# Optimization experiments

Measured on AMD Instinct MI355X. Metric: run time of the kernel, lower is better.

## Reference

```python
import jax, jax.numpy as jnp
import numpy as np

IN_DIM = 128
OUT_DIM = 128
ATTN_DIM = 64
N_REL = 200
N_NODE = 50000
N_EDGE = 500000
N_QUERY = 64
COE_TIMEDIFF = 0.2  # computed in torch code but unused downstream


def setup_inputs() -> dict:
    key = jax.random.key(0)
    ks = jax.random.split(key, 24)
    # edges: [E,7] with columns (r_idx, _, rel, _, tau, sub, obj)
    r_idx = jax.random.randint(ks[0], (N_EDGE,), 0, N_QUERY)
    rel = jax.random.randint(ks[1], (N_EDGE,), 0, 2 * N_REL + 1)
    tau = jax.random.randint(ks[2], (N_EDGE,), -1, 366)  # -1 triggers the where() fallback
    sub = jax.random.randint(ks[3], (N_EDGE,), 0, N_NODE)
    obj = jax.random.randint(ks[4], (N_EDGE,), 0, N_NODE)
    fill = jnp.zeros((N_EDGE,), jnp.int64 if jax.config.jax_enable_x64 else jnp.int32)
    edges = jnp.stack([r_idx, fill, rel, fill, tau, sub, obj], axis=1)
    s = 1.0 / np.sqrt(IN_DIM)
    sa = 1.0 / np.sqrt(ATTN_DIM)
    return {
        "q_sub": jax.random.randint(ks[5], (N_QUERY,), 0, N_NODE),
        "q_rel": jax.random.randint(ks[6], (N_QUERY,), 0, 2 * N_REL + 1),
        "q_tau": jax.random.randint(ks[7], (N_QUERY,), 0, 366),
        "hidden": jax.random.normal(ks[8], (N_NODE, IN_DIM), jnp.float32),
        "edges": edges,
        "n_node": N_NODE,
        "old_nodes_new_idx": jax.random.randint(ks[9], (10000,), 0, N_NODE),
        "rela_embed": jax.random.normal(ks[10], (2 * N_REL + 1, IN_DIM), jnp.float32),
        "Ws": jax.random.normal(ks[11], (IN_DIM, ATTN_DIM), jnp.float32) * s,
        "Wr": jax.random.normal(ks[12], (IN_DIM, ATTN_DIM), jnp.float32) * s,
        "Wqr_W": jax.random.normal(ks[13], (IN_DIM, ATTN_DIM), jnp.float32) * s,
        "Wqr_b": jax.random.normal(ks[14], (ATTN_DIM,), jnp.float32) * s,
        "Wtau": jax.random.normal(ks[15], (IN_DIM, ATTN_DIM), jnp.float32) * s,
        "w_alpha_W": jax.random.normal(ks[16], (ATTN_DIM, 1), jnp.float32) * sa,
        "w_alpha_b": jax.random.normal(ks[17], (1,), jnp.float32) * sa,
        "Wh": jax.random.normal(ks[18], (IN_DIM, OUT_DIM), jnp.float32) * s,
        "wt1": jax.random.normal(ks[19], (1, IN_DIM), jnp.float32),
        "bt1": jax.random.normal(ks[20], (1, IN_DIM), jnp.float32),
        "wt2": jax.random.normal(ks[21], (1, IN_DIM), jnp.float32),
        "bt2": jax.random.normal(ks[22], (1, IN_DIM), jnp.float32),
    }


def reference(q_sub, q_rel, q_tau, hidden, edges, n_node, old_nodes_new_idx,
              rela_embed, Ws, Wr, Wqr_W, Wqr_b, Wtau, w_alpha_W, w_alpha_b,
              Wh, wt1, bt1, wt2, bt2):
    r_idx = edges[:, 0]
    rel = edges[:, 2]
    tau = edges[:, 4]
    sub = edges[:, 5]
    obj = edges[:, 6]
    hs = hidden[sub]                      # [E, in_dim] gather
    hr = rela_embed[rel]                  # [E, in_dim]
    h_qr = rela_embed[q_rel][r_idx]       # [E, in_dim]
    taus_q = q_tau[r_idx]
    tau = jnp.where(tau >= 0, tau, taus_q)
    delta_tau = (tau - taus_q).astype(hidden.dtype)[:, None]  # [E,1]
    h_tau = wt1 * delta_tau + bt1 + jnp.sin(wt2 * delta_tau + bt2)  # [E, in_dim]
    message = hs + hr + h_tau
    pre = jax.nn.relu(hs @ Ws + hr @ Wr + (h_qr @ Wqr_W + Wqr_b) + h_tau @ Wtau)
    alpha = jax.nn.sigmoid(pre @ w_alpha_W + w_alpha_b)  # [E,1]
    msg_agg = jax.ops.segment_sum(alpha * message, obj, num_segments=n_node)
    return msg_agg @ Wh  # act is identity by default
```

## Files before the change

kernel.cpp:

```cpp
#include <hip/hip_runtime.h>
#include <hip/hip_fp16.h>

#define IN_DIM   128
#define OUT_DIM  128
#define ATTN_DIM 64
#define N_RELV   401
#define N_NODE   50000
#define N_EDGE   500000
#define N_QUERY  64
#define N_DT     731
#define CAP      40

typedef unsigned short ushort_t;
typedef unsigned int   uint_t;
typedef __attribute__((ext_vector_type(8))) short v8s;
typedef __attribute__((ext_vector_type(4))) float v4f;

__device__ __forceinline__ int clampi(int v, int lo, int hi) {
    return v < lo ? lo : (v > hi ? hi : v);
}
__device__ __forceinline__ float bu2f(ushort_t u) {
    union { uint_t i; float f; } v; v.i = ((uint_t)u) << 16; return v.f;
}
__device__ __forceinline__ float blo(uint_t u) { return bu2f((ushort_t)(u & 0xffff)); }
__device__ __forceinline__ float bhi(uint_t u) { return bu2f((ushort_t)(u >> 16)); }
__device__ __forceinline__ ushort_t f2bu(float f) {
    union { float f; uint_t i; } v; v.f = f;
    const uint_t x = v.i;
    return (ushort_t)((x + 0x7fffu + ((x >> 16) & 1u)) >> 16);
}

__device__ __forceinline__ void parse_edge(const int* __restrict__ edges, int e,
                                           int i64, int& r, int& rel, int& tau,
                                           int& sub, int& obj) {
    if (i64) {
        const int* E = edges + (size_t)e * 14;
        r = E[0]; rel = E[4]; tau = E[8]; sub = E[10]; obj = E[12];
    } else {
        const int* E = edges + (size_t)e * 7;
        r = E[0]; rel = E[2]; tau = E[4]; sub = E[5]; obj = E[6];
    }
    r   = clampi(r,   0, N_QUERY - 1);
    rel = clampi(rel, 0, N_RELV - 1);
    sub = clampi(sub, 0, N_NODE - 1);
    obj = clampi(obj, 0, N_NODE - 1);
}

__global__ __launch_bounds__(256) void prep_kernel(
    const int* __restrict__ edges, const float* __restrict__ Ws,
    const float* __restrict__ Wh, ushort_t* __restrict__ WTb,
    int* __restrict__ flag, int* __restrict__ cnt, int* __restrict__ ovfn)
{
    const int i = blockIdx.x * 256 + threadIdx.x;
    const int n = i >> 7, k = i & 127;
    const float w = (n < 64) ? Ws[k * 64 + n] : Wh[k * 128 + (n - 64)];
    WTb[i] = f2bu(w);

    for (int idx = i; idx < N_NODE; idx += 96 * 256) cnt[idx] = 0;
    if (i == 0) ovfn[0] = 0;

    if (blockIdx.x == 0) {
        __shared__ int bad;
        if (threadIdx.x == 0) bad = 0;
        __syncthreads();
        for (int t = threadIdx.x; t < 1000; t += 256) {
            const int w32 = edges[2 * t + 1];
            if (w32 != 0 && w32 != -1) bad = 1;
        }
        __syncthreads();
        if (threadIdx.x == 0) flag[0] = (bad == 0) ? 1 : 0;
    }
}

__global__ __launch_bounds__(256) void node_tab_mfma(
    const float* __restrict__ hidden, const ushort_t* __restrict__ WTb,
    ushort_t* __restrict__ node_attn, ushort_t* __restrict__ node_msg)
{
    const int tid  = threadIdx.x;
    const int wid  = tid >> 6;
    const int lane = tid & 63;
    const int m16  = lane & 15;
    const int q    = lane >> 4;
    const int nb   = blockIdx.x * 64;
    const int row  = nb + wid * 16 + m16;
    const int rowc = row < N_NODE ? row : N_NODE - 1;

    v8s hfr[4];
    #pragma unroll
    for (int c = 0; c < 4; ++c) {
        const float4 f0 = *(const float4*)(hidden + (size_t)rowc * 128 + 32 * c + 8 * q);
        const float4 f1 = *(const float4*)(hidden + (size_t)rowc * 128 + 32 * c + 8 * q + 4);
        v8s a;
        a[0] = (short)f2bu(f0.x); a[1] = (short)f2bu(f0.y);
        a[2] = (short)f2bu(f0.z); a[3] = (short)f2bu(f0.w);
        a[4] = (short)f2bu(f1.x); a[5] = (short)f2bu(f1.y);
        a[6] = (short)f2bu(f1.z); a[7] = (short)f2bu(f1.w);
        hfr[c] = a;
    }

    #pragma unroll
    for (int t = 0; t < 12; ++t) {
        v4f acc = {0.f, 0.f, 0.f, 0.f};
        #pragma unroll
        for (int c = 0; c < 4; ++c) {
            const v8s wfr = *(const v8s*)(WTb + (size_t)(16 * t + m16) * 128 + 32 * c + 8 * q);
            acc = __builtin_amdgcn_mfma_f32_16x16x32_bf16(wfr, hfr[c], acc, 0, 0, 0);
        }
        if (row < N_NODE) {
            const uint_t u0 = (uint_t)f2bu(acc[0]) | ((uint_t)f2bu(acc[1]) << 16);
            const uint_t u1 = (uint_t)f2bu(acc[2]) | ((uint_t)f2bu(acc[3]) << 16);
            const int dim = 16 * t + 4 * q;
            if (dim < 64) {
                uint2* dst = (uint2*)(node_attn + (size_t)row * 64 + dim);
                *dst = make_uint2(u0, u1);
            } else {
                uint2* dst = (uint2*)(node_msg + (size_t)row * 128 + (dim - 64));
                *dst = make_uint2(u0, u1);
            }
        }
    }
}

__global__ __launch_bounds__(128) void tables_kernel(
    const float* __restrict__ rela, const float* __restrict__ Wr,
    const float* __restrict__ Wtau, const float* __restrict__ Wh,
    const float* __restrict__ wt1, const float* __restrict__ bt1,
    const float* __restrict__ wt2, const float* __restrict__ bt2,
    const int* __restrict__ q_rel, const float* __restrict__ WqrW,
    const float* __restrict__ Wqrb, const int* __restrict__ flag,
    ushort_t* __restrict__ rel_attn, ushort_t* __restrict__ rel_msg,
    ushort_t* __restrict__ dt_attn,  ushort_t* __restrict__ dt_msg,
    ushort_t* __restrict__ Xqr)
{
    const int b = blockIdx.x, tid = threadIdx.x;
    __shared__ float h[IN_DIM];

    if (b < N_RELV) {
        const int r = b;
        h[tid] = rela[(size_t)r * IN_DIM + tid];
        __syncthreads();
        if (tid < ATTN_DIM) {
            float a = 0.f;
            #pragma unroll 8
            for (int d = 0; d < IN_DIM; ++d) a += h[d] * Wr[d * ATTN_DIM + tid];
            rel_attn[(size_t)r * ATTN_DIM + tid] = f2bu(a);
        }
        float m = 0.f;
        #pragma unroll 8
        for (int d = 0; d < IN_DIM; ++d) m += h[d] * Wh[d * OUT_DIM + tid];
        rel_msg[(size_t)r * OUT_DIM + tid] = f2bu(m);
    } else if (b < N_RELV + N_DT) {
        const int i = b - N_RELV;
        const float dt = (float)(i - 365);
        h[tid] = wt1[tid] * dt + bt1[tid] + sinf(wt2[tid] * dt + bt2[tid]);
        __syncthreads();
        if (tid < ATTN_DIM) {
            float a = 0.f;
            #pragma unroll 8
            for (int d = 0; d < IN_DIM; ++d) a += h[d] * Wtau[d * ATTN_DIM + tid];
            dt_attn[(size_t)i * ATTN_DIM + tid] = f2bu(a);
        }
        float m = 0.f;
        #pragma unroll 8
        for (int d = 0; d < IN_DIM; ++d) m += h[d] * Wh[d * OUT_DIM + tid];
        dt_msg[(size_t)i * OUT_DIM + tid] = f2bu(m);
    } else {
        const int qn  = b - N_RELV - N_DT;
        const int i64 = flag[0];
        const int rel = clampi(q_rel[i64 ? 2 * qn : qn], 0, N_RELV - 1);
        h[tid] = rela[(size_t)rel * IN_DIM + tid];
        __syncthreads();
        if (tid < ATTN_DIM) {
            float acc = Wqrb[tid];
            #pragma unroll 8
            for (int d = 0; d < IN_DIM; ++d) acc += h[d] * WqrW[d * ATTN_DIM + tid];
            Xqr[(size_t)qn * ATTN_DIM + tid] = f2bu(acc);
        }
    }
}

__device__ __forceinline__ float dot8(uint4 xs, uint4 xr, uint4 xt, uint4 xq,
                                      float4 wA, float4 wB)
{
    float s0, s1, v;
    s0 = blo(xs.x) + blo(xr.x) + blo(xt.x) + blo(xq.x);
    s1 = bhi(xs.x) + bhi(xr.x) + bhi(xt.x) + bhi(xq.x);
    v  = fmaxf(s0, 0.f) * wA.x + fmaxf(s1, 0.f) * wA.y;
    s0 = blo(xs.y) + blo(xr.y) + blo(xt.y) + blo(xq.y);
    s1 = bhi(xs.y) + bhi(xr.y) + bhi(xt.y) + bhi(xq.y);
    v += fmaxf(s0, 0.f) * wA.z + fmaxf(s1, 0.f) * wA.w;
    s0 = blo(xs.z) + blo(xr.z) + blo(xt.z) + blo(xq.z);
    s1 = bhi(xs.z) + bhi(xr.z) + bhi(xt.z) + bhi(xq.z);
    v += fmaxf(s0, 0.f) * wB.x + fmaxf(s1, 0.f) * wB.y;
    s0 = blo(xs.w) + blo(xr.w) + blo(xt.w) + blo(xq.w);
    s1 = bhi(xs.w) + bhi(xr.w) + bhi(xt.w) + bhi(xq.w);
    v += fmaxf(s0, 0.f) * wB.z + fmaxf(s1, 0.f) * wB.w;
    return v;
}

__global__ __launch_bounds__(256) void alpha_scatter(
    const int* __restrict__ edges, const int* __restrict__ q_tau,
    const ushort_t* __restrict__ node_attn, const ushort_t* __restrict__ rel_attn,
    const ushort_t* __restrict__ dt_attn,  const ushort_t* __restrict__ Xqr,
    const float* __restrict__ w_alpha_W, const float* __restrict__ w_alpha_b,
    const int* __restrict__ flag, int* __restrict__ cnt,
    int2* __restrict__ meta, int* __restrict__ ovfn, int4* __restrict__ ovfl)
{
    const int g   = threadIdx.x & 7;
    const int grp = threadIdx.x >> 3;
    const int e0  = blockIdx.x * 64 + grp * 2;
    const int i64 = flag[0];

    const float4 wA = *(const float4*)(w_alpha_W + 8 * g);
    const float4 wB = *(const float4*)(w_alpha_W + 8 * g + 4);

    const int ea = e0     < N_EDGE ? e0     : N_EDGE - 1;
    const int eb = e0 + 1 < N_EDGE ? e0 + 1 : N_EDGE - 1;

    int r0, rel0, tau0, sub0, obj0, r1, rel1, tau1, sub1, obj1;
    parse_edge(edges, ea, i64, r0, rel0, tau0, sub0, obj0);
    parse_edge(edges, eb, i64, r1, rel1, tau1, sub1, obj1);
    const int tq0 = q_tau[i64 ? 2 * r0 : r0];
    const int tq1 = q_tau[i64 ? 2 * r1 : r1];
    if (tau0 < 0) tau0 = tq0;
    if (tau1 < 0) tau1 = tq1;
    const int di0 = clampi(tau0 - tq0 + 365, 0, N_DT - 1);
    const int di1 = clampi(tau1 - tq1 + 365, 0, N_DT - 1);

    const uint4 xs0 = *(const uint4*)(node_attn + (size_t)sub0 * ATTN_DIM + 8 * g);
    const uint4 xr0 = *(const uint4*)(rel_attn + (size_t)rel0 * ATTN_DIM + 8 * g);
    const uint4 xt0 = *(const uint4*)(dt_attn  + (size_t)di0  * ATTN_DIM + 8 * g);
    const uint4 xq0 = *(const uint4*)(Xqr      + (size_t)r0   * ATTN_DIM + 8 * g);
    const uint4 xs1 = *(const uint4*)(node_attn + (size_t)sub1 * ATTN_DIM + 8 * g);
    const uint4 xr1 = *(const uint4*)(rel_attn + (size_t)rel1 * ATTN_DIM + 8 * g);
    const uint4 xt1 = *(const uint4*)(dt_attn  + (size_t)di1  * ATTN_DIM + 8 * g);
    const uint4 xq1 = *(const uint4*)(Xqr      + (size_t)r1   * ATTN_DIM + 8 * g);

    float v0 = dot8(xs0, xr0, xt0, xq0, wA, wB);
    float v1 = dot8(xs1, xr1, xt1, xq1, wA, wB);
    v0 += __shfl_down(v0, 4, 8);
    v1 += __shfl_down(v1, 4, 8);
    v0 += __shfl_down(v0, 2, 8);
    v1 += __shfl_down(v1, 2, 8);
    v0 += __shfl_down(v0, 1, 8);
    v1 += __shfl_down(v1, 1, 8);

    if (g == 0) {
        const float wb = w_alpha_b[0];
        if (e0 < N_EDGE) {
            const float alpha = 1.f / (1.f + __expf(-(v0 + wb)));
            const int pos = atomicAdd(&cnt[obj0], 1);
            if (pos < CAP) {
                const uint_t px = (uint_t)sub0 | ((uint_t)di0 << 17) | ((uint_t)(rel0 & 31) << 27);
                const uint_t py = (uint_t)(rel0 >> 5) |
                                  ((uint_t)__half_as_ushort(__float2half_rn(alpha)) << 16);
                meta[(size_t)obj0 * CAP + pos] = make_int2((int)px, (int)py);
            } else {
                const int ov = atomicAdd(ovfn, 1);
                if (ov < N_EDGE)
                    ovfl[ov] = make_int4(sub0 | (di0 << 17), rel0 | (obj0 << 9),
                                         __float_as_int(alpha), 0);
            }
        }
        if (e0 + 1 < N_EDGE) {
            const float alpha = 1.f / (1.f + __expf(-(v1 + wb)));
            const int pos = atomicAdd(&cnt[obj1], 1);
            if (pos < CAP) {
                const uint_t px = (uint_t)sub1 | ((uint_t)di1 << 17) | ((uint_t)(rel1 & 31) << 27);
                const uint_t py = (uint_t)(rel1 >> 5) |
                                  ((uint_t)__half_as_ushort(__float2half_rn(alpha)) << 16);
                meta[(size_t)obj1 * CAP + pos] = make_int2((int)px, (int)py);
            } else {
                const int ov = atomicAdd(ovfn, 1);
                if (ov < N_EDGE)
                    ovfl[ov] = make_int4(sub1 | (di1 << 17), rel1 | (obj1 << 9),
                                         __float_as_int(alpha), 0);
            }
        }
    }
}

__device__ __forceinline__ void meta_decode(int2 m, int& sub, int& di, int& rel,
                                            float& al)
{
    sub = m.x & 0x1FFFF;
    di  = ((uint_t)m.x >> 17) & 0x3FF;
    rel = (((uint_t)m.x >> 27) & 31) | (((uint_t)m.y & 0xF) << 5);
    al  = __half2float(__ushort_as_half((ushort_t)((uint_t)m.y >> 16)));
}

__global__ __launch_bounds__(256) void agg_kernel(
    const int* __restrict__ cnt, const int2* __restrict__ meta,
    const int* __restrict__ ovfn, const int4* __restrict__ ovfl,
    const ushort_t* __restrict__ node_msg, const ushort_t* __restrict__ rel_msg,
    const ushort_t* __restrict__ dt_msg, float* __restrict__ out)
{
    const int lane = threadIdx.x & 63;
    const int n    = blockIdx.x * 4 + (threadIdx.x >> 6);

    int m = cnt[n]; if (m > CAP) m = CAP;
    const int2* row = meta + (size_t)n * CAP;
    float a0 = 0.f, a1 = 0.f;
    int j = 0;
    for (; j + 3 < m; j += 4) {
        const int2 m0 = row[j], m1 = row[j + 1], m2 = row[j + 2], m3 = row[j + 3];
        int s0, d0, r0; float w0; meta_decode(m0, s0, d0, r0, w0);
        int s1, d1, r1; float w1; meta_decode(m1, s1, d1, r1, w1);
        int s2, d2, r2; float w2; meta_decode(m2, s2, d2, r2, w2);
        int s3, d3, r3; float w3; meta_decode(m3, s3, d3, r3, w3);
        const uint_t am0 = *(const uint_t*)(node_msg + (size_t)s0 * 128 + 2 * lane);
        const uint_t bm0 = *(const uint_t*)(rel_msg  + (size_t)r0 * 128 + 2 * lane);
        const uint_t tm0 = *(const uint_t*)(dt_msg   + (size_t)d0 * 128 + 2 * lane);
        const uint_t am1 = *(const uint_t*)(node_msg + (size_t)s1 * 128 + 2 * lane);
        const uint_t bm1 = *(const uint_t*)(rel_msg  + (size_t)r1 * 128 + 2 * lane);
        const uint_t tm1 = *(const uint_t*)(dt_msg   + (size_t)d1 * 128 + 2 * lane);
        const uint_t am2 = *(const uint_t*)(node_msg + (size_t)s2 * 128 + 2 * lane);
        const uint_t bm2 = *(const uint_t*)(rel_msg  + (size_t)r2 * 128 + 2 * lane);
        const uint_t tm2 = *(const uint_t*)(dt_msg   + (size_t)d2 * 128 + 2 * lane);
        const uint_t am3 = *(const uint_t*)(node_msg + (size_t)s3 * 128 + 2 * lane);
        const uint_t bm3 = *(const uint_t*)(rel_msg  + (size_t)r3 * 128 + 2 * lane);
        const uint_t tm3 = *(const uint_t*)(dt_msg   + (size_t)d3 * 128 + 2 * lane);
        a0 += w0 * (blo(am0) + blo(bm0) + blo(tm0));
        a1 += w0 * (bhi(am0) + bhi(bm0) + bhi(tm0));
        a0 += w1 * (blo(am1) + blo(bm1) + blo(tm1));
        a1 += w1 * (bhi(am1) + bhi(bm1) + bhi(tm1));
        a0 += w2 * (blo(am2) + blo(bm2) + blo(tm2));
        a1 += w2 * (bhi(am2) + bhi(bm2) + bhi(tm2));
        a0 += w3 * (blo(am3) + blo(bm3) + blo(tm3));
        a1 += w3 * (bhi(am3) + bhi(bm3) + bhi(tm3));
    }
    for (; j < m; ++j) {
        const int2 m0 = row[j];
        int s0, d0, r0; float w0; meta_decode(m0, s0, d0, r0, w0);
        const uint_t am0 = *(const uint_t*)(node_msg + (size_t)s0 * 128 + 2 * lane);
        const uint_t bm0 = *(const uint_t*)(rel_msg  + (size_t)r0 * 128 + 2 * lane);
        const uint_t tm0 = *(const uint_t*)(dt_msg   + (size_t)d0 * 128 + 2 * lane);
        a0 += w0 * (blo(am0) + blo(bm0) + blo(tm0));
        a1 += w0 * (bhi(am0) + bhi(bm0) + bhi(tm0));
    }

    int nov = ovfn[0]; if (nov > N_EDGE) nov = N_EDGE;
    for (int i = 0; i < nov; ++i) {
        const int4 mo = ovfl[i];
        const int objo = (int)((uint_t)mo.y >> 9);
        if (objo != n) continue;
        const int subo = mo.x & 0x1FFFF;
        const int dio  = (int)((uint_t)mo.x >> 17);
        const int relo = mo.y & 0x1FF;
        const float alo = __int_as_float(mo.z);
        const uint_t am = *(const uint_t*)(node_msg + (size_t)subo * 128 + 2 * lane);
        const uint_t bm = *(const uint_t*)(rel_msg  + (size_t)relo * 128 + 2 * lane);
        const uint_t tm = *(const uint_t*)(dt_msg   + (size_t)dio  * 128 + 2 * lane);
        a0 += alo * (blo(am) + blo(bm) + blo(tm));
        a1 += alo * (bhi(am) + bhi(bm) + bhi(tm));
    }

    ((float2*)(out + (size_t)n * OUT_DIM))[lane] = make_float2(a0, a1);
}

__global__ __launch_bounds__(256) void edge_atomic_kernel(
    const int* __restrict__ edges, const int* __restrict__ q_tau,
    const ushort_t* __restrict__ node_attn, const ushort_t* __restrict__ node_msg,
    const ushort_t* __restrict__ rel_attn,  const ushort_t* __restrict__ rel_msg,
    const ushort_t* __restrict__ dt_attn,   const ushort_t* __restrict__ dt_msg,
    const ushort_t* __restrict__ Xqr,
    const float* __restrict__ w_alpha_W, const float* __restrict__ w_alpha_b,
    const int* __restrict__ flag, float* __restrict__ out)
{
    const int lane = threadIdx.x & 63;
    const int e    = blockIdx.x * 4 + (threadIdx.x >> 6);
    const int i64  = flag[0];

    int r, rel, tau, sub, obj;
    parse_edge(edges, e, i64, r, rel, tau, sub, obj);
    const int tq = q_tau[i64 ? 2 * r : r];
    if (tau < 0) tau = tq;
    const int di = clampi(tau - tq + 365, 0, N_DT - 1);

    const float xs = bu2f(node_attn[(size_t)sub * ATTN_DIM + lane]);
    const float xr = bu2f(rel_attn[(size_t)rel * ATTN_DIM + lane]);
    const float xt = bu2f(dt_attn[(size_t)di  * ATTN_DIM + lane]);
    const float xq = bu2f(Xqr[(size_t)r * ATTN_DIM + lane]);

    float v = fmaxf(xs + xr + xq + xt, 0.f) * w_alpha_W[lane];
    #pragma unroll
    for (int off = 32; off > 0; off >>= 1)
        v += __shfl_down(v, off, 64);
    v = __shfl(v, 0, 64);
    const float alpha = 1.f / (1.f + __expf(-(v + w_alpha_b[0])));

    const uint_t am = *(const uint_t*)(node_msg + (size_t)sub * 128 + 2 * lane);
    const uint_t bm = *(const uint_t*)(rel_msg  + (size_t)rel * 128 + 2 * lane);
    const uint_t tm = *(const uint_t*)(dt_msg   + (size_t)di  * 128 + 2 * lane);
    const float mx = blo(am) + blo(bm) + blo(tm);
    const float my = bhi(am) + bhi(bm) + bhi(tm);

    float* dst = out + (size_t)obj * OUT_DIM;
    atomicAdd(dst + 2 * lane,     alpha * mx);
    atomicAdd(dst + 2 * lane + 1, alpha * my);
}

extern "C" void kernel_launch(void* const* d_in, const int* in_sizes, int n_in,
                              void* d_out, int out_size, void* d_ws, size_t ws_size,
                              hipStream_t stream)
{
    const int*   q_rel  = (const int*)d_in[1];
    const int*   q_tau  = (const int*)d_in[2];
    const float* hidden = (const float*)d_in[3];
    const int*   edges  = (const int*)d_in[4];
    const float* rela   = (const float*)d_in[7];
    const float* Ws     = (const float*)d_in[8];
    const float* Wr     = (const float*)d_in[9];
    const float* WqrW   = (const float*)d_in[10];
    const float* Wqrb   = (const float*)d_in[11];
    const float* Wtau   = (const float*)d_in[12];
    const float* waW    = (const float*)d_in[13];
    const float* wab    = (const float*)d_in[14];
    const float* Wh     = (const float*)d_in[15];
    const float* wt1    = (const float*)d_in[16];
    const float* bt1    = (const float*)d_in[17];
    const float* wt2    = (const float*)d_in[18];
    const float* bt2    = (const float*)d_in[19];
    float* out = (float*)d_out;

    char* p = (char*)d_ws;
    size_t off = 0;
    auto carve = [&](size_t bytes) {
        char* q = p + off;
        off = (off + bytes + 255) & ~(size_t)255;
        return q;
    };
    int*      flag      = (int*)     carve(64);
    int*      cnt       = (int*)     carve((size_t)N_NODE * 4);
    int*      ovfn      = (int*)     carve(64);
    ushort_t* WTb       = (ushort_t*)carve((size_t)192 * 128 * 2);
    ushort_t* XqrB      = (ushort_t*)carve((size_t)N_QUERY * ATTN_DIM * 2);
    ushort_t* rel_attn  = (ushort_t*)carve((size_t)N_RELV * ATTN_DIM * 2);
    ushort_t* rel_msg   = (ushort_t*)carve((size_t)N_RELV * OUT_DIM * 2);
    ushort_t* dt_attn   = (ushort_t*)carve((size_t)N_DT * ATTN_DIM * 2);
    ushort_t* dt_msg    = (ushort_t*)carve((size_t)N_DT * OUT_DIM * 2);
    ushort_t* node_attn = (ushort_t*)carve((size_t)N_NODE * ATTN_DIM * 2);
    ushort_t* node_msg  = (ushort_t*)carve((size_t)N_NODE * OUT_DIM * 2);
    int2*     meta      = (int2*)    carve((size_t)N_NODE * CAP * 8);
    int4*     ovfl      = (int4*)    carve((size_t)N_EDGE * 16);
    const size_t need_full = off;

    prep_kernel<<<96, 256, 0, stream>>>(edges, Ws, Wh, WTb, flag, cnt, ovfn);
    tables_kernel<<<N_RELV + N_DT + N_QUERY, 128, 0, stream>>>(
        rela, Wr, Wtau, Wh, wt1, bt1, wt2, bt2, q_rel, WqrW, Wqrb, flag,
        rel_attn, rel_msg, dt_attn, dt_msg, XqrB);
    node_tab_mfma<<<(N_NODE + 63) / 64, 256, 0, stream>>>(hidden, WTb,
                                                          node_attn, node_msg);

    if (ws_size >= need_full) {
        alpha_scatter<<<(N_EDGE + 63) / 64, 256, 0, stream>>>(
            edges, q_tau, node_attn, rel_attn, dt_attn, XqrB,
            waW, wab, flag, cnt, meta, ovfn, ovfl);
        agg_kernel<<<N_NODE / 4, 256, 0, stream>>>(cnt, meta, ovfn, ovfl,
                                                   node_msg, rel_msg, dt_msg, out);
    } else {
        (void)hipMemsetAsync(out, 0, (size_t)out_size * sizeof(float), stream);
        edge_atomic_kernel<<<N_EDGE / 4, 256, 0, stream>>>(edges, q_tau,
                                                           node_attn, node_msg,
                                                           rel_attn, rel_msg,
                                                           dt_attn, dt_msg, XqrB,
                                                           waW, wab, flag, out);
    }
}
```

Before: 217.1 us.

## Fuse preprocessing kernels, transpose meta layout, widen edge and aggregation work per thread

```diff
diff --git a/kernel.cpp b/kernel.cpp
--- a/kernel.cpp
+++ b/kernel.cpp
@@ -11,6 +11,11 @@
 #define N_DT     731
 #define CAP      40
 
+#define NB_NODE  782
+#define NB_RELDT 566
+#define NB_QR    32
+#define NB_TOT   (NB_NODE + NB_RELDT + NB_QR + 1)
+
 typedef unsigned short ushort_t;
 typedef unsigned int   uint_t;
 typedef __attribute__((ext_vector_type(8))) short v8s;
@@ -28,6 +33,11 @@
     union { float f; uint_t i; } v; v.f = f;
     const uint_t x = v.i;
     return (ushort_t)((x + 0x7fffu + ((x >> 16) & 1u)) >> 16);
+}
+__device__ __forceinline__ uint_t cvtpk(float a, float b) {
+    uint_t r;
+    asm("v_cvt_pk_bf16_f32 %0, %1, %2" : "=v"(r) : "v"(a), "v"(b));
+    return r;
 }
 
 __device__ __forceinline__ void parse_edge(const int* __restrict__ edges, int e,
@@ -46,136 +56,178 @@
     obj = clampi(obj, 0, N_NODE - 1);
 }
 
-__global__ __launch_bounds__(256) void prep_kernel(
-    const int* __restrict__ edges, const float* __restrict__ Ws,
-    const float* __restrict__ Wh, ushort_t* __restrict__ WTb,
+__device__ __forceinline__ int swz_byte(int row, int byte_in_row) {
+    return (row * 256 + byte_in_row) ^ ((row & 7) << 4);
+}
+
+__global__ __launch_bounds__(256) void fused_pre(
+    const float* __restrict__ hidden, const float* __restrict__ Ws,
+    const float* __restrict__ Wh,   const float* __restrict__ rela,
+    const float* __restrict__ Wr,   const float* __restrict__ Wtau,
+    const float* __restrict__ wt1,  const float* __restrict__ bt1,
+    const float* __restrict__ wt2,  const float* __restrict__ bt2,
+    const int* __restrict__ q_rel,  const float* __restrict__ WqrW,
+    const float* __restrict__ Wqrb, const int* __restrict__ edges,
+    ushort_t* __restrict__ node_attn, ushort_t* __restrict__ node_msg,
+    ushort_t* __restrict__ rel_attn,  ushort_t* __restrict__ rel_msg,
+    ushort_t* __restrict__ dt_attn,   ushort_t* __restrict__ dt_msg,
+    ushort_t* __restrict__ Xqr,
     int* __restrict__ flag, int* __restrict__ cnt, int* __restrict__ ovfn)
 {
-    const int i = blockIdx.x * 256 + threadIdx.x;
-    const int n = i >> 7, k = i & 127;
-    const float w = (n < 64) ? Ws[k * 64 + n] : Wh[k * 128 + (n - 64)];
-    WTb[i] = f2bu(w);
-
-    for (int idx = i; idx < N_NODE; idx += 96 * 256) cnt[idx] = 0;
-    if (i == 0) ovfn[0] = 0;
-
-    if (blockIdx.x == 0) {
-        __shared__ int bad;
-        if (threadIdx.x == 0) bad = 0;
-        __syncthreads();
-        for (int t = threadIdx.x; t < 1000; t += 256) {
-            const int w32 = edges[2 * t + 1];
-            if (w32 != 0 && w32 != -1) bad = 1;
-        }
-        __syncthreads();
-        if (threadIdx.x == 0) flag[0] = (bad == 0) ? 1 : 0;
-    }
-}
-
-__global__ __launch_bounds__(256) void node_tab_mfma(
-    const float* __restrict__ hidden, const ushort_t* __restrict__ WTb,
-    ushort_t* __restrict__ node_attn, ushort_t* __restrict__ node_msg)
-{
-    const int tid  = threadIdx.x;
-    const int wid  = tid >> 6;
-    const int lane = tid & 63;
-    const int m16  = lane & 15;
-    const int q    = lane >> 4;
-    const int nb   = blockIdx.x * 64;
-    const int row  = nb + wid * 16 + m16;
-    const int rowc = row < N_NODE ? row : N_NODE - 1;
-
-    v8s hfr[4];
-    #pragma unroll
-    for (int c = 0; c < 4; ++c) {
-        const float4 f0 = *(const float4*)(hidden + (size_t)rowc * 128 + 32 * c + 8 * q);
-        const float4 f1 = *(const float4*)(hidden + (size_t)rowc * 128 + 32 * c + 8 * q + 4);
-        v8s a;
-        a[0] = (short)f2bu(f0.x); a[1] = (short)f2bu(f0.y);
-        a[2] = (short)f2bu(f0.z); a[3] = (short)f2bu(f0.w);
-        a[4] = (short)f2bu(f1.x); a[5] = (short)f2bu(f1.y);
-        a[6] = (short)f2bu(f1.z); a[7] = (short)f2bu(f1.w);
-        hfr[c] = a;
-    }
-
-    #pragma unroll
-    for (int t = 0; t < 12; ++t) {
-        v4f acc = {0.f, 0.f, 0.f, 0.f};
+    __shared__ ushort_t shw[192 * 128];
+    const int bid = blockIdx.x, tid = threadIdx.x;
+
+    if (bid < NB_NODE) {
+        #pragma unroll
+        for (int i = 0; i < 4; ++i) {
+            const int pi = tid + 256 * i;
+            const int kp = pi >> 4;
+            const int n4 = (pi & 15) * 4;
+            const float4 A = *(const float4*)(Ws + (size_t)(2 * kp) * 64 + n4);
+            const float4 B = *(const float4*)(Ws + (size_t)(2 * kp + 1) * 64 + n4);
+            const float Aa[4] = {A.x, A.y, A.z, A.w};
+            const float Bа[4] = {B.x, B.y, B.z, B.w};
+            #pragma unroll
+            for (int j = 0; j < 4; ++j) {
+                const int row = n4 + j;
+                const uint_t u = (uint_t)f2bu(Aa[j]) | ((uint_t)f2bu(Bа[j]) << 16);
+                *(uint_t*)((char*)shw + swz_byte(row, kp * 4)) = u;
+            }
+        }
+        #pragma unroll
+        for (int i = 0; i < 8; ++i) {
+            const int pi = tid + 256 * i;
+            const int kp = pi >> 5;
+            const int n4 = (pi & 31) * 4;
+            const float4 A = *(const float4*)(Wh + (size_t)(2 * kp) * 128 + n4);
+            const float4 B = *(const float4*)(Wh + (size_t)(2 * kp + 1) * 128 + n4);
+            const float Aa[4] = {A.x, A.y, A.z, A.w};
+            const float Bа[4] = {B.x, B.y, B.z, B.w};
+            #pragma unroll
+            for (int j = 0; j < 4; ++j) {
+                const int row = 64 + n4 + j;
+                const uint_t u = (uint_t)f2bu(Aa[j]) | ((uint_t)f2bu(Bа[j]) << 16);
+                *(uint_t*)((char*)shw + swz_byte(row, kp * 4)) = u;
+            }
+        }
+        __syncthreads();
+
+        const int wid  = tid >> 6;
+        const int lane = tid & 63;
+        const int m16  = lane & 15;
+        const int q    = lane >> 4;
+        const int nb   = bid * 64;
+        const int row  = nb + wid * 16 + m16;
+        const int rowc = row < N_NODE ? row : N_NODE - 1;
+
+        v8s hfr[4];
         #pragma unroll
         for (int c = 0; c < 4; ++c) {
-            const v8s wfr = *(const v8s*)(WTb + (size_t)(16 * t + m16) * 128 + 32 * c + 8 * q);
-            acc = __builtin_amdgcn_mfma_f32_16x16x32_bf16(wfr, hfr[c], acc, 0, 0, 0);
-        }
-        if (row < N_NODE) {
-            const uint_t u0 = (uint_t)f2bu(acc[0]) | ((uint_t)f2bu(acc[1]) << 16);
-            const uint_t u1 = (uint_t)f2bu(acc[2]) | ((uint_t)f2bu(acc[3]) << 16);
-            const int dim = 16 * t + 4 * q;
-            if (dim < 64) {
-                uint2* dst = (uint2*)(node_attn + (size_t)row * 64 + dim);
-                *dst = make_uint2(u0, u1);
-            } else {
-                uint2* dst = (uint2*)(node_msg + (size_t)row * 128 + (dim - 64));
-                *dst = make_uint2(u0, u1);
+            const float4 f0 = *(const float4*)(hidden + (size_t)rowc * 128 + 32 * c + 8 * q);
+            const float4 f1 = *(const float4*)(hidden + (size_t)rowc * 128 + 32 * c + 8 * q + 4);
+            union { v8s s; uint4 u; } uu;
+            uu.u = make_uint4(cvtpk(f0.x, f0.y), cvtpk(f0.z, f0.w),
+                              cvtpk(f1.x, f1.y), cvtpk(f1.z, f1.w));
+            hfr[c] = uu.s;
+        }
+
+        #pragma unroll
+        for (int t = 0; t < 12; ++t) {
+            v4f acc = {0.f, 0.f, 0.f, 0.f};
+            #pragma unroll
+            for (int c = 0; c < 4; ++c) {
+                const v8s wfr = *(const v8s*)((const char*)shw +
+                                  swz_byte(16 * t + m16, (32 * c + 8 * q) * 2));
+                acc = __builtin_amdgcn_mfma_f32_16x16x32_bf16(wfr, hfr[c], acc, 0, 0, 0);
             }
-        }
-    }
-}
-
-__global__ __launch_bounds__(128) void tables_kernel(
-    const float* __restrict__ rela, const float* __restrict__ Wr,
-    const float* __restrict__ Wtau, const float* __restrict__ Wh,
-    const float* __restrict__ wt1, const float* __restrict__ bt1,
-    const float* __restrict__ wt2, const float* __restrict__ bt2,
-    const int* __restrict__ q_rel, const float* __restrict__ WqrW,
-    const float* __restrict__ Wqrb, const int* __restrict__ flag,
-    ushort_t* __restrict__ rel_attn, ushort_t* __restrict__ rel_msg,
-    ushort_t* __restrict__ dt_attn,  ushort_t* __restrict__ dt_msg,
-    ushort_t* __restrict__ Xqr)
-{
-    const int b = blockIdx.x, tid = threadIdx.x;
-    __shared__ float h[IN_DIM];
-
-    if (b < N_RELV) {
-        const int r = b;
-        h[tid] = rela[(size_t)r * IN_DIM + tid];
-        __syncthreads();
-        if (tid < ATTN_DIM) {
-            float a = 0.f;
+            if (row < N_NODE) {
+                const uint_t u0 = cvtpk(acc[0], acc[1]);
+                const uint_t u1 = cvtpk(acc[2], acc[3]);
+                const int dim = 16 * t + 4 * q;
+                if (dim < 64) {
+                    *(uint2*)(node_attn + (size_t)row * 64 + dim) = make_uint2(u0, u1);
+                } else {
+                    *(uint2*)(node_msg + (size_t)row * 128 + (dim - 64)) = make_uint2(u0, u1);
+                }
+            }
+        }
+    } else if (bid < NB_NODE + NB_RELDT) {
+        const int bid2   = bid - NB_NODE;
+        const int half   = tid >> 7;
+        const int t128   = tid & 127;
+        const int rowid  = bid2 * 2 + half;
+        float* h = (float*)shw + half * 128;
+
+        if (rowid < N_RELV) {
+            h[t128] = rela[(size_t)rowid * IN_DIM + t128];
+        } else {
+            const float dtv = (float)((rowid - N_RELV) - 365);
+            h[t128] = wt1[t128] * dtv + bt1[t128] + sinf(wt2[t128] * dtv + bt2[t128]);
+        }
+        __syncthreads();
+
+        if (rowid < N_RELV) {
+            if (t128 < ATTN_DIM) {
+                float a = 0.f;
+                #pragma unroll 8
+                for (int d = 0; d < IN_DIM; ++d) a += h[d] * Wr[d * ATTN_DIM + t128];
+                rel_attn[(size_t)rowid * ATTN_DIM + t128] = f2bu(a);
+            }
+            float m = 0.f;
             #pragma unroll 8
-            for (int d = 0; d < IN_DIM; ++d) a += h[d] * Wr[d * ATTN_DIM + tid];
-            rel_attn[(size_t)r * ATTN_DIM + tid] = f2bu(a);
-        }
-        float m = 0.f;
-        #pragma unroll 8
-        for (int d = 0; d < IN_DIM; ++d) m += h[d] * Wh[d * OUT_DIM + tid];
-        rel_msg[(size_t)r * OUT_DIM + tid] = f2bu(m);
-    } else if (b < N_RELV + N_DT) {
-        const int i = b - N_RELV;
-        const float dt = (float)(i - 365);
-        h[tid] = wt1[tid] * dt + bt1[tid] + sinf(wt2[tid] * dt + bt2[tid]);
-        __syncthreads();
-        if (tid < ATTN_DIM) {
-            float a = 0.f;
+            for (int d = 0; d < IN_DIM; ++d) m += h[d] * Wh[d * OUT_DIM + t128];
+            rel_msg[(size_t)rowid * OUT_DIM + t128] = f2bu(m);
+        } else {
+            const int i = rowid - N_RELV;
+            if (t128 < ATTN_DIM) {
+                float a = 0.f;
+                #pragma unroll 8
+                for (int d = 0; d < IN_DIM; ++d) a += h[d] * Wtau[d * ATTN_DIM + t128];
+                dt_attn[(size_t)i * ATTN_DIM + t128] = f2bu(a);
+            }
+            float m = 0.f;
             #pragma unroll 8
-            for (int d = 0; d < IN_DIM; ++d) a += h[d] * Wtau[d * ATTN_DIM + tid];
-            dt_attn[(size_t)i * ATTN_DIM + tid] = f2bu(a);
-        }
-        float m = 0.f;
-        #pragma unroll 8
-        for (int d = 0; d < IN_DIM; ++d) m += h[d] * Wh[d * OUT_DIM + tid];
-        dt_msg[(size_t)i * OUT_DIM + tid] = f2bu(m);
+            for (int d = 0; d < IN_DIM; ++d) m += h[d] * Wh[d * OUT_DIM + t128];
+            dt_msg[(size_t)i * OUT_DIM + t128] = f2bu(m);
+        }
+        const int z = bid2 * 89 + tid;
+        if (tid < 89 && z < N_NODE) cnt[z] = 0;
+    } else if (bid < NB_NODE + NB_RELDT + NB_QR) {
+        const int bid3 = bid - NB_NODE - NB_RELDT;
+        const int half = tid >> 7;
+        const int t128 = tid & 127;
+        float* h  = (float*)shw + half * 128;
+        int*   ok = (int*)((float*)shw + 512);
+
+        if (tid == 0) *ok = 1;
+        __syncthreads();
+        const int w = edges[2 * tid + 1];
+        if (w != 0 && w != -1) *ok = 0;
+        __syncthreads();
+        const int i64 = *ok;
+
+        const int qn  = bid3 * 2 + half;
+        const int rel = clampi(q_rel[i64 ? 2 * qn : qn], 0, N_RELV - 1);
+        h[t128] = rela[(size_t)rel * IN_DIM + t128];
+        __syncthreads();
+        if (t128 < ATTN_DIM) {
+            float acc = Wqrb[t128];
+            #pragma unroll 8
+            for (int d = 0; d < IN_DIM; ++d) acc += h[d] * WqrW[d * ATTN_DIM + t128];
+            Xqr[(size_t)qn * ATTN_DIM + t128] = f2bu(acc);
+        }
     } else {
-        const int qn  = b - N_RELV - N_DT;
-        const int i64 = flag[0];
-        const int rel = clampi(q_rel[i64 ? 2 * qn : qn], 0, N_RELV - 1);
-        h[tid] = rela[(size_t)rel * IN_DIM + tid];
-        __syncthreads();
-        if (tid < ATTN_DIM) {
-            float acc = Wqrb[tid];
-            #pragma unroll 8
-            for (int d = 0; d < IN_DIM; ++d) acc += h[d] * WqrW[d * ATTN_DIM + tid];
-            Xqr[(size_t)qn * ATTN_DIM + tid] = f2bu(acc);
-        }
+        int* ok = (int*)shw;
+        if (tid == 0) *ok = 0;
+        __syncthreads();
+        int badv = 0;
+        for (int t = tid; t < 1000; t += 256) {
+            const int w = edges[2 * t + 1];
+            if (w != 0 && w != -1) badv = 1;
+        }
+        if (badv) *ok = 1;
+        __syncthreads();
+        if (tid == 0) { flag[0] = (*ok == 0) ? 1 : 0; ovfn[0] = 0; }
     }
 }
 
@@ -208,24 +260,33 @@
 {
     const int g   = threadIdx.x & 7;
     const int grp = threadIdx.x >> 3;
-    const int e0  = blockIdx.x * 64 + grp * 2;
+    const int e0  = blockIdx.x * 128 + grp * 4;
     const int i64 = flag[0];
 
     const float4 wA = *(const float4*)(w_alpha_W + 8 * g);
     const float4 wB = *(const float4*)(w_alpha_W + 8 * g + 4);
 
-    const int ea = e0     < N_EDGE ? e0     : N_EDGE - 1;
-    const int eb = e0 + 1 < N_EDGE ? e0 + 1 : N_EDGE - 1;
-
-    int r0, rel0, tau0, sub0, obj0, r1, rel1, tau1, sub1, obj1;
-    parse_edge(edges, ea, i64, r0, rel0, tau0, sub0, obj0);
-    parse_edge(edges, eb, i64, r1, rel1, tau1, sub1, obj1);
+    const int ec0 = e0     < N_EDGE ? e0     : N_EDGE - 1;
+    const int ec1 = e0 + 1 < N_EDGE ? e0 + 1 : N_EDGE - 1;
+    const int ec2 = e0 + 2 < N_EDGE ? e0 + 2 : N_EDGE - 1;
+    const int ec3 = e0 + 3 < N_EDGE ? e0 + 3 : N_EDGE - 1;
+
+    int r0, rel0, tau0, sub0, obj0; parse_edge(edges, ec0, i64, r0, rel0, tau0, sub0, obj0);
+    int r1, rel1, tau1, sub1, obj1; parse_edge(edges, ec1, i64, r1, rel1, tau1, sub1, obj1);
+    int r2, rel2, tau2, sub2, obj2; parse_edge(edges, ec2, i64, r2, rel2, tau2, sub2, obj2);
+    int r3, rel3, tau3, sub3, obj3; parse_edge(edges, ec3, i64, r3, rel3, tau3, sub3, obj3);
     const int tq0 = q_tau[i64 ? 2 * r0 : r0];
     const int tq1 = q_tau[i64 ? 2 * r1 : r1];
+    const int tq2 = q_tau[i64 ? 2 * r2 : r2];
+    const int tq3 = q_tau[i64 ? 2 * r3 : r3];
     if (tau0 < 0) tau0 = tq0;
     if (tau1 < 0) tau1 = tq1;
+    if (tau2 < 0) tau2 = tq2;
+    if (tau3 < 0) tau3 = tq3;
     const int di0 = clampi(tau0 - tq0 + 365, 0, N_DT - 1);
     const int di1 = clampi(tau1 - tq1 + 365, 0, N_DT - 1);
+    const int di2 = clampi(tau2 - tq2 + 365, 0, N_DT - 1);
+    const int di3 = clampi(tau3 - tq3 + 365, 0, N_DT - 1);
 
     const uint4 xs0 = *(const uint4*)(node_attn + (size_t)sub0 * ATTN_DIM + 8 * g);
     const uint4 xr0 = *(const uint4*)(rel_attn + (size_t)rel0 * ATTN_DIM + 8 * g);
@@ -235,58 +296,67 @@
     const uint4 xr1 = *(const uint4*)(rel_attn + (size_t)rel1 * ATTN_DIM + 8 * g);
     const uint4 xt1 = *(const uint4*)(dt_attn  + (size_t)di1  * ATTN_DIM + 8 * g);
     const uint4 xq1 = *(const uint4*)(Xqr      + (size_t)r1   * ATTN_DIM + 8 * g);
+    const uint4 xs2 = *(const uint4*)(node_attn + (size_t)sub2 * ATTN_DIM + 8 * g);
+    const uint4 xr2 = *(const uint4*)(rel_attn + (size_t)rel2 * ATTN_DIM + 8 * g);
+    const uint4 xt2 = *(const uint4*)(dt_attn  + (size_t)di2  * ATTN_DIM + 8 * g);
+    const uint4 xq2 = *(const uint4*)(Xqr      + (size_t)r2   * ATTN_DIM + 8 * g);
+    const uint4 xs3 = *(const uint4*)(node_attn + (size_t)sub3 * ATTN_DIM + 8 * g);
+    const uint4 xr3 = *(const uint4*)(rel_attn + (size_t)rel3 * ATTN_DIM + 8 * g);
+    const uint4 xt3 = *(const uint4*)(dt_attn  + (size_t)di3  * ATTN_DIM + 8 * g);
+    const uint4 xq3 = *(const uint4*)(Xqr      + (size_t)r3   * ATTN_DIM + 8 * g);
 
     float v0 = dot8(xs0, xr0, xt0, xq0, wA, wB);
     float v1 = dot8(xs1, xr1, xt1, xq1, wA, wB);
-    v0 += __shfl_down(v0, 4, 8);
-    v1 += __shfl_down(v1, 4, 8);
-    v0 += __shfl_down(v0, 2, 8);
-    v1 += __shfl_down(v1, 2, 8);
-    v0 += __shfl_down(v0, 1, 8);
-    v1 += __shfl_down(v1, 1, 8);
-
-    if (g == 0) {
-        const float wb = w_alpha_b[0];
-        if (e0 < N_EDGE) {
-            const float alpha = 1.f / (1.f + __expf(-(v0 + wb)));
-            const int pos = atomicAdd(&cnt[obj0], 1);
-            if (pos < CAP) {
-                const uint_t px = (uint_t)sub0 | ((uint_t)di0 << 17) | ((uint_t)(rel0 & 31) << 27);
-                const uint_t py = (uint_t)(rel0 >> 5) |
-                                  ((uint_t)__half_as_ushort(__float2half_rn(alpha)) << 16);
-                meta[(size_t)obj0 * CAP + pos] = make_int2((int)px, (int)py);
-            } else {
-                const int ov = atomicAdd(ovfn, 1);
-                if (ov < N_EDGE)
-                    ovfl[ov] = make_int4(sub0 | (di0 << 17), rel0 | (obj0 << 9),
-                                         __float_as_int(alpha), 0);
-            }
-        }
-        if (e0 + 1 < N_EDGE) {
-            const float alpha = 1.f / (1.f + __expf(-(v1 + wb)));
-            const int pos = atomicAdd(&cnt[obj1], 1);
-            if (pos < CAP) {
-                const uint_t px = (uint_t)sub1 | ((uint_t)di1 << 17) | ((uint_t)(rel1 & 31) << 27);
-                const uint_t py = (uint_t)(rel1 >> 5) |
-                                  ((uint_t)__half_as_ushort(__float2half_rn(alpha)) << 16);
-                meta[(size_t)obj1 * CAP + pos] = make_int2((int)px, (int)py);
-            } else {
-                const int ov = atomicAdd(ovfn, 1);
-                if (ov < N_EDGE)
-                    ovfl[ov] = make_int4(sub1 | (di1 << 17), rel1 | (obj1 << 9),
-                                         __float_as_int(alpha), 0);
-            }
-        }
-    }
-}
-
-__device__ __forceinline__ void meta_decode(int2 m, int& sub, int& di, int& rel,
-                                            float& al)
-{
-    sub = m.x & 0x1FFFF;
-    di  = ((uint_t)m.x >> 17) & 0x3FF;
-    rel = (((uint_t)m.x >> 27) & 31) | (((uint_t)m.y & 0xF) << 5);
-    al  = __half2float(__ushort_as_half((ushort_t)((uint_t)m.y >> 16)));
+    float v2 = dot8(xs2, xr2, xt2, xq2, wA, wB);
+    float v3 = dot8(xs3, xr3, xt3, xq3, wA, wB);
+
+    #pragma unroll
+    for (int off = 4; off > 0; off >>= 1) {
+        v0 += __shfl_xor(v0, off, 8);
+        v1 += __shfl_xor(v1, off, 8);
+        v2 += __shfl_xor(v2, off, 8);
+        v3 += __shfl_xor(v3, off, 8);
+    }
+
+    if (g < 4 && e0 + g < N_EDGE) {
+        const float vg  = g == 0 ? v0 : (g == 1 ? v1 : (g == 2 ? v2 : v3));
+        const int objg  = g == 0 ? obj0 : (g == 1 ? obj1 : (g == 2 ? obj2 : obj3));
+        const int subg  = g == 0 ? sub0 : (g == 1 ? sub1 : (g == 2 ? sub2 : sub3));
+        const int dig   = g == 0 ? di0  : (g == 1 ? di1  : (g == 2 ? di2  : di3));
+        const int relg  = g == 0 ? rel0 : (g == 1 ? rel1 : (g == 2 ? rel2 : rel3));
+        const float alpha = 1.f / (1.f + __expf(-(vg + w_alpha_b[0])));
+        const int pos = atomicAdd(&cnt[objg], 1);
+        if (pos < CAP) {
+            const uint_t px = (uint_t)subg | ((uint_t)dig << 17) | ((uint_t)(relg & 31) << 27);
+            const uint_t py = (uint_t)(relg >> 5) |
+                              ((uint_t)__half_as_ushort(__float2half_rn(alpha)) << 16);
+            meta[(size_t)pos * N_NODE + objg] = make_int2((int)px, (int)py);
+        } else {
+            const int ov = atomicAdd(ovfn, 1);
+            if (ov < N_EDGE)
+                ovfl[ov] = make_int4(subg | (dig << 17), relg | (objg << 9),
+                                     __float_as_int(alpha), 0);
+        }
+    }
+}
+
+__device__ __forceinline__ void agg_edge(
+    int2 m, int l32,
+    const ushort_t* __restrict__ node_msg, const ushort_t* __restrict__ rel_msg,
+    const ushort_t* __restrict__ dt_msg,
+    float& a0, float& a1, float& a2, float& a3)
+{
+    const int sub = m.x & 0x1FFFF;
+    const int di  = ((uint_t)m.x >> 17) & 0x3FF;
+    const int rel = (((uint_t)m.x >> 27) & 31) | (((uint_t)m.y & 0xF) << 5);
+    const float al = __half2float(__ushort_as_half((ushort_t)((uint_t)m.y >> 16)));
+    const uint2 am = *(const uint2*)(node_msg + (size_t)sub * 128 + 4 * l32);
+    const uint2 bm = *(const uint2*)(rel_msg  + (size_t)rel * 128 + 4 * l32);
+    const uint2 tm = *(const uint2*)(dt_msg   + (size_t)di  * 128 + 4 * l32);
+    a0 += al * (blo(am.x) + blo(bm.x) + blo(tm.x));
+    a1 += al * (bhi(am.x) + bhi(bm.x) + bhi(tm.x));
+    a2 += al * (blo(am.y) + blo(bm.y) + blo(tm.y));
+    a3 += al * (bhi(am.y) + bhi(bm.y) + bhi(tm.y));
 }
 
 __global__ __launch_bounds__(256) void agg_kernel(
@@ -296,66 +366,56 @@
     const ushort_t* __restrict__ dt_msg, float* __restrict__ out)
 {
     const int lane = threadIdx.x & 63;
+    const int half = lane >> 5;
+    const int l32  = lane & 31;
     const int n    = blockIdx.x * 4 + (threadIdx.x >> 6);
 
     int m = cnt[n]; if (m > CAP) m = CAP;
-    const int2* row = meta + (size_t)n * CAP;
-    float a0 = 0.f, a1 = 0.f;
+    float a0 = 0.f, a1 = 0.f, a2 = 0.f, a3 = 0.f;
+
     int j = 0;
     for (; j + 3 < m; j += 4) {
-        const int2 m0 = row[j], m1 = row[j + 1], m2 = row[j + 2], m3 = row[j + 3];
-        int s0, d0, r0; float w0; meta_decode(m0, s0, d0, r0, w0);
-        int s1, d1, r1; float w1; meta_decode(m1, s1, d1, r1, w1);
-        int s2, d2, r2; float w2; meta_decode(m2, s2, d2, r2, w2);
-        int s3, d3, r3; float w3; meta_decode(m3, s3, d3, r3, w3);
-        const uint_t am0 = *(const uint_t*)(node_msg + (size_t)s0 * 128 + 2 * lane);
-        const uint_t bm0 = *(const uint_t*)(rel_msg  + (size_t)r0 * 128 + 2 * lane);
-        const uint_t tm0 = *(const uint_t*)(dt_msg   + (size_t)d0 * 128 + 2 * lane);
-        const uint_t am1 = *(const uint_t*)(node_msg + (size_t)s1 * 128 + 2 * lane);
-        const uint_t bm1 = *(const uint_t*)(rel_msg  + (size_t)r1 * 128 + 2 * lane);
-        const uint_t tm1 = *(const uint_t*)(dt_msg   + (size_t)d1 * 128 + 2 * lane);
-        const uint_t am2 = *(const uint_t*)(node_msg + (size_t)s2 * 128 + 2 * lane);
-        const uint_t bm2 = *(const uint_t*)(rel_msg  + (size_t)r2 * 128 + 2 * lane);
-        const uint_t tm2 = *(const uint_t*)(dt_msg   + (size_t)d2 * 128 + 2 * lane);
-        const uint_t am3 = *(const uint_t*)(node_msg + (size_t)s3 * 128 + 2 * lane);
-        const uint_t bm3 = *(const uint_t*)(rel_msg  + (size_t)r3 * 128 + 2 * lane);
-        const uint_t tm3 = *(const uint_t*)(dt_msg   + (size_t)d3 * 128 + 2 * lane);
-        a0 += w0 * (blo(am0) + blo(bm0) + blo(tm0));
-        a1 += w0 * (bhi(am0) + bhi(bm0) + bhi(tm0));
-        a0 += w1 * (blo(am1) + blo(bm1) + blo(tm1));
-        a1 += w1 * (bhi(am1) + bhi(bm1) + bhi(tm1));
-        a0 += w2 * (blo(am2) + blo(bm2) + blo(tm2));
-        a1 += w2 * (bhi(am2) + bhi(bm2) + bhi(tm2));
-        a0 += w3 * (blo(am3) + blo(bm3) + blo(tm3));
-        a1 += w3 * (bhi(am3) + bhi(bm3) + bhi(tm3));
-    }
-    for (; j < m; ++j) {
-        const int2 m0 = row[j];
-        int s0, d0, r0; float w0; meta_decode(m0, s0, d0, r0, w0);
-        const uint_t am0 = *(const uint_t*)(node_msg + (size_t)s0 * 128 + 2 * lane);
-        const uint_t bm0 = *(const uint_t*)(rel_msg  + (size_t)r0 * 128 + 2 * lane);
-        const uint_t tm0 = *(const uint_t*)(dt_msg   + (size_t)d0 * 128 + 2 * lane);
-        a0 += w0 * (blo(am0) + blo(bm0) + blo(tm0));
-        a1 += w0 * (bhi(am0) + bhi(bm0) + bhi(tm0));
+        const int2 ma = meta[(size_t)(j + half) * N_NODE + n];
+        const int2 mb = meta[(size_t)(j + 2 + half) * N_NODE + n];
+        agg_edge(ma, l32, node_msg, rel_msg, dt_msg, a0, a1, a2, a3);
+        agg_edge(mb, l32, node_msg, rel_msg, dt_msg, a0, a1, a2, a3);
+    }
+    for (; j + 1 < m; j += 2) {
+        const int2 ma = meta[(size_t)(j + half) * N_NODE + n];
+        agg_edge(ma, l32, node_msg, rel_msg, dt_msg, a0, a1, a2, a3);
+    }
+    if (j < m && half == 0) {
+        const int2 ma = meta[(size_t)j * N_NODE + n];
+        agg_edge(ma, l32, node_msg, rel_msg, dt_msg, a0, a1, a2, a3);
     }
 
     int nov = ovfn[0]; if (nov > N_EDGE) nov = N_EDGE;
     for (int i = 0; i < nov; ++i) {
         const int4 mo = ovfl[i];
         const int objo = (int)((uint_t)mo.y >> 9);
-        if (objo != n) continue;
+        if (objo != n || half != 0) continue;
         const int subo = mo.x & 0x1FFFF;
         const int dio  = (int)((uint_t)mo.x >> 17);
         const int relo = mo.y & 0x1FF;
         const float alo = __int_as_float(mo.z);
-        const uint_t am = *(const uint_t*)(node_msg + (size_t)subo * 128 + 2 * lane);
-        const uint_t bm = *(const uint_t*)(rel_msg  + (size_t)relo * 128 + 2 * lane);
-        const uint_t tm = *(const uint_t*)(dt_msg   + (size_t)dio  * 128 + 2 * lane);
-        a0 += alo * (blo(am) + blo(bm) + blo(tm));
-        a1 += alo * (bhi(am) + bhi(bm) + bhi(tm));
-    }
-
-    ((float2*)(out + (size_t)n * OUT_DIM))[lane] = make_float2(a0, a1);
+        const uint2 am = *(const uint2*)(node_msg + (size_t)subo * 128 + 4 * l32);
+        const uint2 bm = *(const uint2*)(rel_msg  + (size_t)relo * 128 + 4 * l32);
+        const uint2 tm = *(const uint2*)(dt_msg   + (size_t)dio  * 128 + 4 * l32);
+        a0 += alo * (blo(am.x) + blo(bm.x) + blo(tm.x));
+        a1 += alo * (bhi(am.x) + bhi(bm.x) + bhi(tm.x));
+        a2 += alo * (blo(am.y) + blo(bm.y) + blo(tm.y));
+        a3 += alo * (bhi(am.y) + bhi(bm.y) + bhi(tm.y));
+    }
+
+    a0 += __shfl_xor(a0, 32, 64);
+    a1 += __shfl_xor(a1, 32, 64);
+    a2 += __shfl_xor(a2, 32, 64);
+    a3 += __shfl_xor(a3, 32, 64);
+
+    if (half == 0) {
+        float4 o; o.x = a0; o.y = a1; o.z = a2; o.w = a3;
+        *(float4*)(out + (size_t)n * OUT_DIM + 4 * l32) = o;
+    }
 }
 
 __global__ __launch_bounds__(256) void edge_atomic_kernel(
@@ -433,7 +493,6 @@
     int*      flag      = (int*)     carve(64);
     int*      cnt       = (int*)     carve((size_t)N_NODE * 4);
     int*      ovfn      = (int*)     carve(64);
-    ushort_t* WTb       = (ushort_t*)carve((size_t)192 * 128 * 2);
     ushort_t* XqrB      = (ushort_t*)carve((size_t)N_QUERY * ATTN_DIM * 2);
     ushort_t* rel_attn  = (ushort_t*)carve((size_t)N_RELV * ATTN_DIM * 2);
     ushort_t* rel_msg   = (ushort_t*)carve((size_t)N_RELV * OUT_DIM * 2);
@@ -445,15 +504,14 @@
     int4*     ovfl      = (int4*)    carve((size_t)N_EDGE * 16);
     const size_t need_full = off;
 
-    prep_kernel<<<96, 256, 0, stream>>>(edges, Ws, Wh, WTb, flag, cnt, ovfn);
-    tables_kernel<<<N_RELV + N_DT + N_QUERY, 128, 0, stream>>>(
-        rela, Wr, Wtau, Wh, wt1, bt1, wt2, bt2, q_rel, WqrW, Wqrb, flag,
-        rel_attn, rel_msg, dt_attn, dt_msg, XqrB);
-    node_tab_mfma<<<(N_NODE + 63) / 64, 256, 0, stream>>>(hidden, WTb,
-                                                          node_attn, node_msg);
+    fused_pre<<<NB_TOT, 256, 0, stream>>>(
+        hidden, Ws, Wh, rela, Wr, Wtau, wt1, bt1, wt2, bt2,
+        q_rel, WqrW, Wqrb, edges,
+        node_attn, node_msg, rel_attn, rel_msg, dt_attn, dt_msg, XqrB,
+        flag, cnt, ovfn);
 
     if (ws_size >= need_full) {
-        alpha_scatter<<<(N_EDGE + 63) / 64, 256, 0, stream>>>(
+        alpha_scatter<<<(N_EDGE + 127) / 128, 256, 0, stream>>>(
             edges, q_tau, node_attn, rel_attn, dt_attn, XqrB,
             waW, wab, flag, cnt, meta, ovfn, ovfl);
         agg_kernel<<<N_NODE / 4, 256, 0, stream>>>(cnt, meta, ovfn, ovfl,
```

After: 200.2 us. -7.8%, faster.
